# Performance work log

Hardware: AMD Instinct MI355X
Metric: run time of the kernel (lower is better)

Reference implementation:

```python
import jax, jax.numpy as jnp
import numpy as np

D = 12      # depth
C = 768     # embed_dim
NH = 12     # num_heads
P = 16      # patch_size
IMG = 224
G = IMG // P          # 14 patch grid
N = G * G + 1         # 197 tokens (CLS + patches)
WIN = 7               # window_size
NC = 1000             # num_classes
HID = 3072            # mlp hidden


def _local_mask():
    m = np.zeros((N, N), dtype=bool)
    m[0, :] = True
    m[:, 0] = True
    idx = np.arange(N - 1)
    r = idx // G
    c = idx % G
    half = WIN // 2
    m[1:, 1:] = (np.abs(r[:, None] - r[None, :]) <= half) & (np.abs(c[:, None] - c[None, :]) <= half)
    return jnp.asarray(m)

MASK = _local_mask()


def _ln(x, w, b, eps=1e-5):
    mu = x.mean(-1, keepdims=True)
    var = ((x - mu) ** 2).mean(-1, keepdims=True)
    return (x - mu) / jnp.sqrt(var + eps) * w + b


def setup_inputs() -> dict:
    key = jax.random.key(0)
    ks = jax.random.split(key, 16)
    s = jnp.float32(0.02)
    B = 32
    return {
        "x": jax.random.normal(ks[0], (B, 3, IMG, IMG), jnp.float32),
        "patch_w": jax.random.normal(ks[1], (C, 3, P, P), jnp.float32) * s,
        "patch_b": jnp.zeros((C,), jnp.float32),
        "cls_token": jax.random.normal(ks[2], (1, 1, C), jnp.float32) * s,
        "pos_embed": jax.random.normal(ks[3], (1, N, C), jnp.float32) * s,
        "ln1_w": jnp.ones((D, C), jnp.float32),
        "ln1_b": jnp.zeros((D, C), jnp.float32),
        "qkv_w": jax.random.normal(ks[4], (D, C, 3 * C), jnp.float32) * s,
        "proj_w": jax.random.normal(ks[5], (D, C, C), jnp.float32) * s,
        "proj_b": jnp.zeros((D, C), jnp.float32),
        "ln2_w": jnp.ones((D, C), jnp.float32),
        "ln2_b": jnp.zeros((D, C), jnp.float32),
        "mlp_w1": jax.random.normal(ks[6], (D, C, HID), jnp.float32) * s,
        "mlp_b1": jnp.zeros((D, HID), jnp.float32),
        "mlp_w2": jax.random.normal(ks[7], (D, HID, C), jnp.float32) * s,
        "mlp_b2": jnp.zeros((D, C), jnp.float32),
        "norm_w": jnp.ones((C,), jnp.float32),
        "norm_b": jnp.zeros((C,), jnp.float32),
        "head_w": jax.random.normal(ks[8], (C, NC), jnp.float32) * s,
        "head_b": jnp.zeros((NC,), jnp.float32),
    }


def reference(x, patch_w, patch_b, cls_token, pos_embed, ln1_w, ln1_b, qkv_w,
              proj_w, proj_b, ln2_w, ln2_b, mlp_w1, mlp_b1, mlp_w2, mlp_b2,
              norm_w, norm_b, head_w, head_b):
    B = x.shape[0]
    hd = C // NH
    scale = hd ** -0.5
    # Patch embed (Conv2d stride=kernel == non-overlapping patch matmul)
    xp = x.reshape(B, 3, G, P, G, P).transpose(0, 2, 4, 1, 3, 5).reshape(B, G * G, 3 * P * P)
    t = xp @ patch_w.reshape(C, 3 * P * P).T + patch_b
    t = jnp.concatenate([jnp.broadcast_to(cls_token, (B, 1, C)), t], axis=1) + pos_embed
    for i in range(D):
        h = _ln(t, ln1_w[i], ln1_b[i])
        qkv = (h @ qkv_w[i]).reshape(B, N, 3, NH, hd)
        q, k, v = qkv[:, :, 0], qkv[:, :, 1], qkv[:, :, 2]  # (B,N,NH,hd)
        attn = jnp.einsum('bqhd,bkhd->bhqk', q, k) * scale
        attn = jnp.where(MASK, attn, -jnp.inf)
        attn = jax.nn.softmax(attn, axis=-1)
        o = jnp.einsum('bhqk,bkhd->bqhd', attn, v).reshape(B, N, C)
        t = t + o @ proj_w[i] + proj_b[i]
        h = _ln(t, ln2_w[i], ln2_b[i])
        h = jax.nn.gelu(h @ mlp_w1[i] + mlp_b1[i], approximate=False)
        t = t + h @ mlp_w2[i] + mlp_b2[i]
    t = _ln(t, norm_w, norm_b)
    return t[:, 0] @ head_w + head_b
```

## Files before the change

### kernel.cpp

```cpp
#include <hip/hip_runtime.h>
#include <hip/hip_bf16.h>
#include <math.h>

#define Dn 12
#define Cc 768
#define NHh 12
#define HD 64
#define Gg 14
#define Nn_TOK 197
#define HID 3072
#define NC 1000
#define Bb 32

typedef __attribute__((ext_vector_type(8))) short short8;
typedef __attribute__((ext_vector_type(4))) float f32x4;

__device__ __forceinline__ ushort f2b(float v) {
    union { float f; unsigned u; } x; x.f = v;
    unsigned r = x.u + 0x7fff + ((x.u >> 16) & 1);
    return (ushort)(r >> 16);
}
__device__ __forceinline__ float b2f(ushort v) {
    union { unsigned u; float f; } x; x.u = ((unsigned)v) << 16; return x.f;
}
__device__ __forceinline__ void gld16(const void* g, void* s) {
    __builtin_amdgcn_global_load_lds(
        (const __attribute__((address_space(1))) void*)g,
        (__attribute__((address_space(3))) void*)s, 16, 0, 0);
}

__global__ void im2col_kernel(const float* __restrict__ x, ushort* __restrict__ xp) {
    size_t idx = (size_t)blockIdx.x * 256 + threadIdx.x;
    const size_t total = (size_t)Bb * 196 * 768;
    if (idx >= total) return;
    int j = idx % 768;
    size_t t0 = idx / 768;
    int g = t0 % 196;
    int b = t0 / 196;
    int ch = j / 256, rem = j % 256, pr = rem / 16, pc = rem % 16;
    int gr = g / Gg, gc = g % Gg;
    int row = gr * 16 + pr, col = gc * 16 + pc;
    xp[idx] = f2b(x[(((size_t)b * 3 + ch) * 224 + row) * 224 + col]);
}

__global__ void assemble_kernel(const float* __restrict__ pe, const float* __restrict__ cls,
                                const float* __restrict__ pos, float* __restrict__ t) {
    size_t idx = (size_t)blockIdx.x * 256 + threadIdx.x;
    const size_t total = (size_t)Bb * Nn_TOK * 768;
    if (idx >= total) return;
    int c = idx % 768;
    size_t r = idx / 768;
    int n = r % Nn_TOK, b = r / Nn_TOK;
    float v;
    if (n == 0) v = cls[c];
    else       v = pe[((size_t)b * 196 + (n - 1)) * 768 + c];
    t[idx] = v + pos[(size_t)n * 768 + c];
}

__global__ void cvt_kernel(const float* __restrict__ src, ushort* __restrict__ dst, int n) {
    int idx = blockIdx.x * 256 + threadIdx.x;
    if (idx < n) dst[idx] = f2b(src[idx]);
}

__global__ __launch_bounds__(256) void transpose_one(const float* __restrict__ src,
                                                     ushort* __restrict__ dst, int K, int N) {
    int k0 = blockIdx.x * 32, n0 = blockIdx.y * 32;
    __shared__ float tile[32][33];
    int tx = threadIdx.x & 31, ty = threadIdx.x >> 5;
    #pragma unroll
    for (int r = ty; r < 32; r += 8)
        if (k0 + r < K && n0 + tx < N)
            tile[r][tx] = src[(size_t)(k0 + r) * N + n0 + tx];
    __syncthreads();
    #pragma unroll
    for (int r = ty; r < 32; r += 8)
        if (n0 + r < N && k0 + tx < K)
            dst[(size_t)(n0 + r) * K + k0 + tx] = f2b(tile[tx][r]);
}

__global__ __launch_bounds__(256) void transpose4_kernel(
    const float* __restrict__ qkvw, const float* __restrict__ projw,
    const float* __restrict__ w1, const float* __restrict__ w2,
    ushort* __restrict__ dq, ushort* __restrict__ dp,
    ushort* __restrict__ d1, ushort* __restrict__ d2)
{
    int tile = blockIdx.x;
    const float* src; ushort* dst; int N, kt, nt;
    if (tile < 1728)      { src = qkvw; dst = dq; N = 2304; kt = tile / 72; nt = tile % 72; }
    else if (tile < 2304) { tile -= 1728; src = projw; dst = dp; N = 768; kt = tile / 24; nt = tile % 24; }
    else if (tile < 4608) { tile -= 2304; src = w1; dst = d1; N = 3072; kt = tile / 96; nt = tile % 96; }
    else                  { tile -= 4608; src = w2; dst = d2; N = 768; kt = tile / 24; nt = tile % 24; }
    int K = (dst == d2) ? 3072 : 768;
    int k0 = kt * 32, n0 = nt * 32;
    __shared__ float tilebuf[32][33];
    int tx = threadIdx.x & 31, ty = threadIdx.x >> 5;
    #pragma unroll
    for (int r = ty; r < 32; r += 8)
        tilebuf[r][tx] = src[(size_t)(k0 + r) * N + n0 + tx];
    __syncthreads();
    #pragma unroll
    for (int r = ty; r < 32; r += 8)
        dst[(size_t)(n0 + r) * K + k0 + tx] = f2b(tilebuf[tx][r]);
}

#define TM 128
#define TN 128
__global__ __launch_bounds__(256) void gemm_bf16(
    const ushort* __restrict__ A, const ushort* __restrict__ B,
    void* __restrict__ outp, const float* __restrict__ bias,
    const float* __restrict__ residual, int M, int N, int K, int flags)
{
    __shared__ ushort As[2][4][128][8];
    __shared__ ushort Bs[2][4][128][8];
    const int tid = threadIdx.x;
    const int wave = tid >> 6, lane = tid & 63;

    const int nwg = gridDim.x * gridDim.y;
    const int orig = blockIdx.y * gridDim.x + blockIdx.x;
    const int xcd = orig & 7, loc = orig >> 3;
    const int q8 = nwg >> 3, r8 = nwg & 7;
    const int swz = (xcd < r8 ? xcd * (q8 + 1) : r8 * (q8 + 1) + (xcd - r8) * q8) + loc;
    const int bx = swz % gridDim.x, by = swz / gridDim.x;

    const int br = by * TM, bc = bx * TN;
    const int wm = (wave >> 1) * 64, wn = (wave & 1) * 64;

    const int hA0 = tid >> 7, rA0 = tid & 127;
    const int hA1 = (tid + 256) >> 7;
    const ushort* pA0 = A + (size_t)min(br + rA0, M - 1) * K + hA0 * 8;
    const ushort* pA1 = A + (size_t)min(br + rA0, M - 1) * K + hA1 * 8;
    const ushort* pB0 = B + (size_t)min(bc + rA0, N - 1) * K + hA0 * 8;
    const ushort* pB1 = B + (size_t)min(bc + rA0, N - 1) * K + hA1 * 8;
    ushort* sA0 = &As[0][0][0][0] + (size_t)(wave * 64) * 8;
    ushort* sA1 = &As[0][0][0][0] + (size_t)(256 + wave * 64) * 8;
    ushort* sB0 = &Bs[0][0][0][0] + (size_t)(wave * 64) * 8;
    ushort* sB1 = &Bs[0][0][0][0] + (size_t)(256 + wave * 64) * 8;
    const size_t BUFO = 4096;

    f32x4 acc[4][4];
    #pragma unroll
    for (int i = 0; i < 4; ++i)
        #pragma unroll
        for (int j = 0; j < 4; ++j) acc[i][j] = (f32x4){0.f, 0.f, 0.f, 0.f};

    const int h = lane >> 4, m16 = lane & 15;
    const int nk = K >> 5;

    gld16(pA0, sA0); gld16(pA1, sA1);
    gld16(pB0, sB0); gld16(pB1, sB1);

    for (int kt = 0; kt < nk; ++kt) {
        const int cur = kt & 1;
        if (kt + 1 < nk) {
            const size_t ko = (size_t)(kt + 1) * 32;
            const size_t bo = (size_t)((kt + 1) & 1) * BUFO;
            gld16(pA0 + ko, sA0 + bo); gld16(pA1 + ko, sA1 + bo);
            gld16(pB0 + ko, sB0 + bo); gld16(pB1 + ko, sB1 + bo);
            asm volatile("s_waitcnt vmcnt(4)" ::: "memory");
        } else {
            asm volatile("s_waitcnt vmcnt(0)" ::: "memory");
        }
        __builtin_amdgcn_s_barrier();

        short8 af[4], bfr[4];
        #pragma unroll
        for (int i = 0; i < 4; ++i) af[i]  = *(const short8*)&As[cur][h][wm + i * 16 + m16][0];
        #pragma unroll
        for (int j = 0; j < 4; ++j) bfr[j] = *(const short8*)&Bs[cur][h][wn + j * 16 + m16][0];
        #pragma unroll
        for (int i = 0; i < 4; ++i)
            #pragma unroll
            for (int j = 0; j < 4; ++j)
                acc[i][j] = __builtin_amdgcn_mfma_f32_16x16x32_bf16(af[i], bfr[j], acc[i][j], 0, 0, 0);

        asm volatile("s_waitcnt lgkmcnt(0)" ::: "memory");
        __builtin_amdgcn_sched_barrier(0);
        __builtin_amdgcn_s_barrier();
    }

    const bool obf = (flags & 2) != 0, gelu = (flags & 1) != 0;
    const int q = lane >> 4, cx = lane & 15;
    #pragma unroll
    for (int j = 0; j < 4; ++j) {
        int gc = bc + wn + j * 16 + cx;
        if (gc >= N) continue;
        float bv = bias ? bias[gc] : 0.f;
        #pragma unroll
        for (int i = 0; i < 4; ++i) {
            #pragma unroll
            for (int r = 0; r < 4; ++r) {
                int gr = br + wm + i * 16 + q * 4 + r;
                if (gr >= M) continue;
                float v = acc[i][j][r] + bv;
                if (gelu) v = 0.5f * v * (1.f + erff(v * 0.70710678118654752f));
                size_t off = (size_t)gr * N + gc;
                if (residual) v += residual[off];
                if (obf) ((ushort*)outp)[off] = f2b(v);
                else     ((float*)outp)[off] = v;
            }
        }
    }
}

__global__ __launch_bounds__(256) void ln_kernel(
    const float* __restrict__ in, ushort* __restrict__ out,
    const float* __restrict__ w, const float* __restrict__ b, long in_stride)
{
    int row = blockIdx.x;
    const float* xr = in + (size_t)row * in_stride;
    ushort* orow = out + (size_t)row * 768;
    int tid = threadIdx.x;
    float vals[3];
    float s = 0.f, s2 = 0.f;
    #pragma unroll
    for (int l = 0; l < 3; ++l) {
        float v = xr[tid + l * 256];
        vals[l] = v; s += v; s2 += v * v;
    }
    __shared__ float sh[256];
    __shared__ float stats[2];
    sh[tid] = s; __syncthreads();
    for (int o = 128; o > 0; o >>= 1) { if (tid < o) sh[tid] += sh[tid + o]; __syncthreads(); }
    if (tid == 0) stats[0] = sh[0];
    __syncthreads();
    sh[tid] = s2; __syncthreads();
    for (int o = 128; o > 0; o >>= 1) { if (tid < o) sh[tid] += sh[tid + o]; __syncthreads(); }
    if (tid == 0) stats[1] = sh[0];
    __syncthreads();
    float mean = stats[0] * (1.f / 768.f);
    float var = stats[1] * (1.f / 768.f) - mean * mean;
    float rstd = rsqrtf(var + 1e-5f);
    #pragma unroll
    for (int l = 0; l < 3; ++l) {
        int c = tid + l * 256;
        orow[c] = f2b((vals[l] - mean) * rstd * w[c] + b[c]);
    }
}

#define VST 232
__global__ __launch_bounds__(256) void attn_kernel(
    const ushort* __restrict__ qkv, ushort* __restrict__ out)
{
    const int h = blockIdx.x, b = blockIdx.y, zs = blockIdx.z;
    __shared__ ushort Vsh[64][VST];
    __shared__ ushort Psh[4][16][VST];
    const int tid = threadIdx.x, wave = tid >> 6, lane = tid & 63;
    const size_t base = (size_t)b * Nn_TOK * 2304 + (size_t)h * 64;

    {
        short8* vf = (short8*)&Vsh[0][0];
        for (int i = tid; i < 64 * VST / 8; i += 256)
            vf[i] = (short8){0, 0, 0, 0, 0, 0, 0, 0};
    }
    __syncthreads();
    for (int idx = tid; idx < Nn_TOK * 32; idx += 256) {
        int n = idx >> 5, d2 = (idx & 31) * 2;
        unsigned u = *(const unsigned*)(qkv + base + 1536 + (size_t)n * 2304 + d2);
        Vsh[d2][n]     = (ushort)(u & 0xffffu);
        Vsh[d2 + 1][n] = (ushort)(u >> 16);
    }
    *(unsigned long long*)&Psh[wave][lane >> 2][208 + (lane & 3) * 4] = 0ull;
    __syncthreads();

    const int kcol = lane & 15, lhi = lane >> 4;
    int rk[14], ck[14]; bool kin[14], kwin[14];
    #pragma unroll
    for (int kt = 0; kt < 14; ++kt) {
        int k = kt * 16 + kcol;
        kin[kt]  = (k < Nn_TOK);
        kwin[kt] = (k >= 1) && (k < Nn_TOK);
        int km1 = k - 1;
        rk[kt] = km1 / 14;
        ck[kt] = km1 - rk[kt] * 14;
    }
    const bool kcls = (kcol == 0);

    const int tlo = zs ? 7 : 0, thi = zs ? 13 : 7;
    for (int qt = tlo + wave; qt < thi; qt += 4) {
        const int qbase = qt * 16;
        const int qrow = qbase + kcol;
        const ushort* qp = qkv + base + (size_t)min(qrow, Nn_TOK - 1) * 2304 + lhi * 8;
        const short8 qf0 = *(const short8*)qp;
        const short8 qf1 = *(const short8*)(qp + 32);

        f32x4 S[14];
        #pragma unroll
        for (int kt = 0; kt < 14; ++kt) {
            int krow = min(kt * 16 + kcol, Nn_TOK - 1);
            const ushort* kp = qkv + base + 768 + (size_t)krow * 2304 + lhi * 8;
            short8 kf0 = *(const short8*)kp;
            short8 kf1 = *(const short8*)(kp + 32);
            f32x4 s = (f32x4){0.f, 0.f, 0.f, 0.f};
            s = __builtin_amdgcn_mfma_f32_16x16x32_bf16(qf0, kf0, s, 0, 0, 0);
            s = __builtin_amdgcn_mfma_f32_16x16x32_bf16(qf1, kf1, s, 0, 0, 0);
            S[kt] = s;
        }

        int rq_[4], cq_[4]; bool qc_[4];
        #pragma unroll
        for (int r = 0; r < 4; ++r) {
            int q = qbase + lhi * 4 + r;
            qc_[r] = (q == 0);
            int qm1 = q - 1;
            rq_[r] = qm1 / 14;
            cq_[r] = qm1 - rq_[r] * 14;
        }
        #pragma unroll
        for (int kt = 0; kt < 14; ++kt)
            #pragma unroll
            for (int r = 0; r < 4; ++r) {
                unsigned dr = (unsigned)(rq_[r] - rk[kt] + 3);
                unsigned dc = (unsigned)(cq_[r] - ck[kt] + 3);
                bool ok = (kwin[kt] && dr <= 6u && dc <= 6u)
                          || (qc_[r] && kin[kt]) || (kt == 0 && kcls);
                S[kt][r] = ok ? S[kt][r] : -1e30f;
            }

        float mx[4] = {-1e30f, -1e30f, -1e30f, -1e30f};
        #pragma unroll
        for (int kt = 0; kt < 14; ++kt)
            #pragma unroll
            for (int r = 0; r < 4; ++r) mx[r] = fmaxf(mx[r], S[kt][r]);
        #pragma unroll
        for (int r = 0; r < 4; ++r) {
            #pragma unroll
            for (int o = 8; o > 0; o >>= 1) mx[r] = fmaxf(mx[r], __shfl_xor(mx[r], o));
        }
        float ls[4] = {0.f, 0.f, 0.f, 0.f};
        #pragma unroll
        for (int kt = 0; kt < 14; ++kt)
            #pragma unroll
            for (int r = 0; r < 4; ++r) {
                float p = __expf((S[kt][r] - mx[r]) * 0.125f);
                S[kt][r] = p; ls[r] += p;
            }
        #pragma unroll
        for (int r = 0; r < 4; ++r) {
            #pragma unroll
            for (int o = 8; o > 0; o >>= 1) ls[r] += __shfl_xor(ls[r], o);
            ls[r] = 1.f / ls[r];
        }

        #pragma unroll
        for (int kt = 0; kt < 13; ++kt)
            #pragma unroll
            for (int r = 0; r < 4; ++r)
                Psh[wave][lhi * 4 + r][kt * 16 + kcol] = f2b(S[kt][r] * ls[r]);

        f32x4 O[4];
        #pragma unroll
        for (int j = 0; j < 4; ++j) O[j] = (f32x4){0.f, 0.f, 0.f, 0.f};
        #pragma unroll
        for (int ks = 0; ks < 7; ++ks) {
            short8 pf = *(const short8*)&Psh[wave][kcol][ks * 32 + lhi * 8];
            #pragma unroll
            for (int j = 0; j < 4; ++j) {
                short8 vfr = *(const short8*)&Vsh[j * 16 + kcol][ks * 32 + lhi * 8];
                O[j] = __builtin_amdgcn_mfma_f32_16x16x32_bf16(pf, vfr, O[j], 0, 0, 0);
            }
        }

        #pragma unroll
        for (int r = 0; r < 4; ++r) {
            int q = qbase + lhi * 4 + r;
            if (q < Nn_TOK) {
                size_t orow = ((size_t)b * Nn_TOK + q) * 768 + (size_t)h * 64;
                #pragma unroll
                for (int j = 0; j < 4; ++j)
                    out[orow + j * 16 + kcol] = f2b(O[j][r]);
            }
        }
    }
}

extern "C" void kernel_launch(void* const* d_in, const int* in_sizes, int n_in,
                              void* d_out, int out_size, void* d_ws, size_t ws_size,
                              hipStream_t stream) {
    const float* x        = (const float*)d_in[0];
    const float* patch_w  = (const float*)d_in[1];
    const float* patch_b  = (const float*)d_in[2];
    const float* cls_tok  = (const float*)d_in[3];
    const float* pos_emb  = (const float*)d_in[4];
    const float* ln1_w    = (const float*)d_in[5];
    const float* ln1_b    = (const float*)d_in[6];
    const float* qkv_w    = (const float*)d_in[7];
    const float* proj_w   = (const float*)d_in[8];
    const float* proj_b   = (const float*)d_in[9];
    const float* ln2_w    = (const float*)d_in[10];
    const float* ln2_b    = (const float*)d_in[11];
    const float* mlp_w1   = (const float*)d_in[12];
    const float* mlp_b1   = (const float*)d_in[13];
    const float* mlp_w2   = (const float*)d_in[14];
    const float* mlp_b2   = (const float*)d_in[15];
    const float* norm_w   = (const float*)d_in[16];
    const float* norm_b   = (const float*)d_in[17];
    const float* head_w   = (const float*)d_in[18];
    const float* head_b   = (const float*)d_in[19];
    float* out = (float*)d_out;

    char* ws = (char*)d_ws;
    float*  t     = (float*)ws;
    float*  pbuf  = (float*)(ws + 19365888);
    ushort* abuf  = (ushort*)(ws + 38633472);
    ushort* qbuf  = (ushort*)(ws + 48316416);
    ushort* hbuf  = (ushort*)(ws + 77365248);
    ushort* wq    = (ushort*)(ws + 116097024);
    ushort* wp    = wq + 1769472;
    ushort* w1t   = wp + 589824;
    ushort* w2t   = w1t + 2359296;
    ushort* pwbuf = (ushort*)(ws + 130252800);
    ushort* hwbuf = (ushort*)(ws + 131432448);

    const int M_tok = Bb * Nn_TOK;

    {
        size_t total = (size_t)Bb * 196 * 768;
        im2col_kernel<<<dim3((total + 255) / 256), 256, 0, stream>>>(x, abuf);
    }
    cvt_kernel<<<dim3((589824 + 255) / 256), 256, 0, stream>>>(patch_w, pwbuf, 589824);
    transpose_one<<<dim3(24, 32), 256, 0, stream>>>(head_w, hwbuf, 768, NC);
    gemm_bf16<<<dim3(6, 49), 256, 0, stream>>>(abuf, pwbuf, pbuf, patch_b, nullptr, Bb * 196, Cc, Cc, 0);
    {
        size_t total = (size_t)M_tok * 768;
        assemble_kernel<<<dim3((total + 255) / 256), 256, 0, stream>>>(pbuf, cls_tok, pos_emb, t);
    }

    for (int i = 0; i < Dn; ++i) {
        transpose4_kernel<<<dim3(6912), 256, 0, stream>>>(
            qkv_w + (size_t)i * Cc * 3 * Cc, proj_w + (size_t)i * Cc * Cc,
            mlp_w1 + (size_t)i * Cc * HID, mlp_w2 + (size_t)i * HID * Cc,
            wq, wp, w1t, w2t);
        ln_kernel<<<dim3(M_tok), 256, 0, stream>>>(t, abuf, ln1_w + i * Cc, ln1_b + i * Cc, Cc);
        gemm_bf16<<<dim3(18, 50), 256, 0, stream>>>(abuf, wq, qbuf, nullptr, nullptr, M_tok, 3 * Cc, Cc, 2);
        attn_kernel<<<dim3(NHh, Bb, 2), 256, 0, stream>>>(qbuf, abuf);
        gemm_bf16<<<dim3(6, 50), 256, 0, stream>>>(abuf, wp, t, proj_b + i * Cc, t, M_tok, Cc, Cc, 0);
        ln_kernel<<<dim3(M_tok), 256, 0, stream>>>(t, abuf, ln2_w + i * Cc, ln2_b + i * Cc, Cc);
        gemm_bf16<<<dim3(24, 50), 256, 0, stream>>>(abuf, w1t, hbuf, mlp_b1 + i * HID, nullptr, M_tok, HID, Cc, 3);
        gemm_bf16<<<dim3(6, 50), 256, 0, stream>>>(hbuf, w2t, t, mlp_b2 + i * Cc, t, M_tok, Cc, HID, 0);
    }

    ln_kernel<<<dim3(Bb), 256, 0, stream>>>(t, abuf, norm_w, norm_b, (long)Nn_TOK * Cc);
    gemm_bf16<<<dim3(8, 1), 256, 0, stream>>>(abuf, hwbuf, out, head_b, nullptr, Bb, NC, Cc, 0);
}
```

Baseline: 5.474 ms.

## Replace 128x128 GEMM with templated 256xBN tile, K=64 steps, swizzled LDS

Replaces the 256-thread 128x128 bf16 MFMA GEMM with a templated 512-thread kernel. It uses 256-row tiles, 128- or 256-column tiles and a K step of 64, with an XOR-swizzled shared-memory layout and s_setprio around the MFMA bursts. The goals are more reuse per loaded tile, fewer barriers per K, and fewer LDS bank conflicts. In exchange it uses more registers and LDS, and some GEMMs launch fewer workgroups, for example 150 blocks for the N=768 GEMMs, which may underfill the GPU.

After: 4.817 ms. -12.0%, faster.

```diff
diff --git a/kernel.cpp b/kernel.cpp
--- a/kernel.cpp
+++ b/kernel.cpp
@@ -103,17 +103,22 @@
         dst[(size_t)(n0 + r) * K + k0 + tx] = f2b(tilebuf[tx][r]);
 }
 
-#define TM 128
-#define TN 128
-__global__ __launch_bounds__(256) void gemm_bf16(
+template<int BN>
+__global__ __launch_bounds__(512, 2) void gemm_t(
     const ushort* __restrict__ A, const ushort* __restrict__ B,
     void* __restrict__ outp, const float* __restrict__ bias,
     const float* __restrict__ residual, int M, int N, int K, int flags)
 {
-    __shared__ ushort As[2][4][128][8];
-    __shared__ ushort Bs[2][4][128][8];
+    constexpr int JF = BN / 64;
+    constexpr int BI = BN / 64;
+    constexpr int ATILE = 256 * 64;
+    constexpr int BTILE = BN * 64;
+    __shared__ ushort As[2 * ATILE];
+    __shared__ ushort Bs[2 * BTILE];
+
     const int tid = threadIdx.x;
     const int wave = tid >> 6, lane = tid & 63;
+    const int wr = wave >> 2, wc = wave & 3;
 
     const int nwg = gridDim.x * gridDim.y;
     const int orig = blockIdx.y * gridDim.x + blockIdx.x;
@@ -121,78 +126,98 @@
     const int q8 = nwg >> 3, r8 = nwg & 7;
     const int swz = (xcd < r8 ? xcd * (q8 + 1) : r8 * (q8 + 1) + (xcd - r8) * q8) + loc;
     const int bx = swz % gridDim.x, by = swz / gridDim.x;
-
-    const int br = by * TM, bc = bx * TN;
-    const int wm = (wave >> 1) * 64, wn = (wave & 1) * 64;
-
-    const int hA0 = tid >> 7, rA0 = tid & 127;
-    const int hA1 = (tid + 256) >> 7;
-    const ushort* pA0 = A + (size_t)min(br + rA0, M - 1) * K + hA0 * 8;
-    const ushort* pA1 = A + (size_t)min(br + rA0, M - 1) * K + hA1 * 8;
-    const ushort* pB0 = B + (size_t)min(bc + rA0, N - 1) * K + hA0 * 8;
-    const ushort* pB1 = B + (size_t)min(bc + rA0, N - 1) * K + hA1 * 8;
-    ushort* sA0 = &As[0][0][0][0] + (size_t)(wave * 64) * 8;
-    ushort* sA1 = &As[0][0][0][0] + (size_t)(256 + wave * 64) * 8;
-    ushort* sB0 = &Bs[0][0][0][0] + (size_t)(wave * 64) * 8;
-    ushort* sB1 = &Bs[0][0][0][0] + (size_t)(256 + wave * 64) * 8;
-    const size_t BUFO = 4096;
-
-    f32x4 acc[4][4];
-    #pragma unroll
-    for (int i = 0; i < 4; ++i)
-        #pragma unroll
-        for (int j = 0; j < 4; ++j) acc[i][j] = (f32x4){0.f, 0.f, 0.f, 0.f};
-
-    const int h = lane >> 4, m16 = lane & 15;
-    const int nk = K >> 5;
-
-    gld16(pA0, sA0); gld16(pA1, sA1);
-    gld16(pB0, sB0); gld16(pB1, sB1);
-
-    for (int kt = 0; kt < nk; ++kt) {
-        const int cur = kt & 1;
-        if (kt + 1 < nk) {
-            const size_t ko = (size_t)(kt + 1) * 32;
-            const size_t bo = (size_t)((kt + 1) & 1) * BUFO;
-            gld16(pA0 + ko, sA0 + bo); gld16(pA1 + ko, sA1 + bo);
-            gld16(pB0 + ko, sB0 + bo); gld16(pB1 + ko, sB1 + bo);
-            asm volatile("s_waitcnt vmcnt(4)" ::: "memory");
+    const int br = by * 256, bc = bx * BN;
+
+    const int srow = lane >> 3;
+    const int sswz = (lane & 7) ^ srow;
+    const ushort* pA[4]; const ushort* pB[4];
+    ushort* sA[4]; ushort* sB[4];
+    #pragma unroll
+    for (int i = 0; i < 4; ++i) {
+        int row = i * 64 + wave * 8 + srow;
+        pA[i] = A + (size_t)min(br + row, M - 1) * K + sswz * 8;
+        sA[i] = As + (i * 64 + wave * 8) * 64;
+    }
+    #pragma unroll
+    for (int i = 0; i < BI; ++i) {
+        int row = i * 64 + wave * 8 + srow;
+        pB[i] = B + (size_t)min(bc + row, N - 1) * K + sswz * 8;
+        sB[i] = Bs + (i * 64 + wave * 8) * 64;
+    }
+
+    f32x4 acc[8][JF];
+    #pragma unroll
+    for (int i = 0; i < 8; ++i)
+        #pragma unroll
+        for (int j = 0; j < JF; ++j) acc[i][j] = (f32x4){0.f, 0.f, 0.f, 0.f};
+
+    const int m16 = lane & 15, h = lane >> 4;
+    const int arow = (wr * 128 + m16) * 64;
+    const int brow = (wc * (BN / 4) + m16) * 64;
+    const int sx = m16 & 7;
+
+    const int nt = K >> 6;
+    #pragma unroll
+    for (int i = 0; i < 4; ++i) gld16(pA[i], sA[i]);
+    #pragma unroll
+    for (int i = 0; i < BI; ++i) gld16(pB[i], sB[i]);
+
+    for (int t = 0; t < nt; ++t) {
+        const int cur = t & 1;
+        if (t + 1 < nt) {
+            const size_t ko = (size_t)(t + 1) << 6;
+            const int nxt = cur ^ 1;
+            #pragma unroll
+            for (int i = 0; i < 4; ++i) gld16(pA[i] + ko, sA[i] + nxt * ATILE);
+            #pragma unroll
+            for (int i = 0; i < BI; ++i) gld16(pB[i] + ko, sB[i] + nxt * BTILE);
+            if constexpr (BN == 256) asm volatile("s_waitcnt vmcnt(8)" ::: "memory");
+            else                     asm volatile("s_waitcnt vmcnt(6)" ::: "memory");
         } else {
             asm volatile("s_waitcnt vmcnt(0)" ::: "memory");
         }
         __builtin_amdgcn_s_barrier();
-
-        short8 af[4], bfr[4];
-        #pragma unroll
-        for (int i = 0; i < 4; ++i) af[i]  = *(const short8*)&As[cur][h][wm + i * 16 + m16][0];
-        #pragma unroll
-        for (int j = 0; j < 4; ++j) bfr[j] = *(const short8*)&Bs[cur][h][wn + j * 16 + m16][0];
-        #pragma unroll
-        for (int i = 0; i < 4; ++i)
-            #pragma unroll
-            for (int j = 0; j < 4; ++j)
-                acc[i][j] = __builtin_amdgcn_mfma_f32_16x16x32_bf16(af[i], bfr[j], acc[i][j], 0, 0, 0);
-
+        __builtin_amdgcn_sched_barrier(0);
+
+        const ushort* Abase = As + cur * ATILE;
+        const ushort* Bbase = Bs + cur * BTILE;
+        #pragma unroll
+        for (int ks = 0; ks < 2; ++ks) {
+            const int slot = (((ks << 2) | h) ^ sx) << 3;
+            short8 af[8], bf[JF];
+            #pragma unroll
+            for (int i = 0; i < 8; ++i)
+                af[i] = *(const short8*)(Abase + arow + i * 1024 + slot);
+            #pragma unroll
+            for (int j = 0; j < JF; ++j)
+                bf[j] = *(const short8*)(Bbase + brow + j * 1024 + slot);
+            __builtin_amdgcn_s_setprio(1);
+            #pragma unroll
+            for (int i = 0; i < 8; ++i)
+                #pragma unroll
+                for (int j = 0; j < JF; ++j)
+                    acc[i][j] = __builtin_amdgcn_mfma_f32_16x16x32_bf16(af[i], bf[j], acc[i][j], 0, 0, 0);
+            __builtin_amdgcn_s_setprio(0);
+        }
         asm volatile("s_waitcnt lgkmcnt(0)" ::: "memory");
         __builtin_amdgcn_sched_barrier(0);
         __builtin_amdgcn_s_barrier();
     }
 
-    const bool obf = (flags & 2) != 0, gelu = (flags & 1) != 0;
-    const int q = lane >> 4, cx = lane & 15;
-    #pragma unroll
-    for (int j = 0; j < 4; ++j) {
-        int gc = bc + wn + j * 16 + cx;
+    const bool obf = (flags & 2) != 0, geluf = (flags & 1) != 0;
+    #pragma unroll
+    for (int j = 0; j < JF; ++j) {
+        int gc = bc + wc * (BN / 4) + j * 16 + m16;
         if (gc >= N) continue;
         float bv = bias ? bias[gc] : 0.f;
         #pragma unroll
-        for (int i = 0; i < 4; ++i) {
+        for (int i = 0; i < 8; ++i) {
             #pragma unroll
             for (int r = 0; r < 4; ++r) {
-                int gr = br + wm + i * 16 + q * 4 + r;
+                int gr = br + wr * 128 + i * 16 + h * 4 + r;
                 if (gr >= M) continue;
                 float v = acc[i][j][r] + bv;
-                if (gelu) v = 0.5f * v * (1.f + erff(v * 0.70710678118654752f));
+                if (geluf) v = 0.5f * v * (1.f + erff(v * 0.70710678118654752f));
                 size_t off = (size_t)gr * N + gc;
                 if (residual) v += residual[off];
                 if (obf) ((ushort*)outp)[off] = f2b(v);
@@ -419,7 +444,7 @@
     }
     cvt_kernel<<<dim3((589824 + 255) / 256), 256, 0, stream>>>(patch_w, pwbuf, 589824);
     transpose_one<<<dim3(24, 32), 256, 0, stream>>>(head_w, hwbuf, 768, NC);
-    gemm_bf16<<<dim3(6, 49), 256, 0, stream>>>(abuf, pwbuf, pbuf, patch_b, nullptr, Bb * 196, Cc, Cc, 0);
+    gemm_t<128><<<dim3(6, 25), 512, 0, stream>>>(abuf, pwbuf, pbuf, patch_b, nullptr, Bb * 196, Cc, Cc, 0);
     {
         size_t total = (size_t)M_tok * 768;
         assemble_kernel<<<dim3((total + 255) / 256), 256, 0, stream>>>(pbuf, cls_tok, pos_emb, t);
@@ -431,14 +456,14 @@
             mlp_w1 + (size_t)i * Cc * HID, mlp_w2 + (size_t)i * HID * Cc,
             wq, wp, w1t, w2t);
         ln_kernel<<<dim3(M_tok), 256, 0, stream>>>(t, abuf, ln1_w + i * Cc, ln1_b + i * Cc, Cc);
-        gemm_bf16<<<dim3(18, 50), 256, 0, stream>>>(abuf, wq, qbuf, nullptr, nullptr, M_tok, 3 * Cc, Cc, 2);
+        gemm_t<256><<<dim3(9, 25), 512, 0, stream>>>(abuf, wq, qbuf, nullptr, nullptr, M_tok, 3 * Cc, Cc, 2);
         attn_kernel<<<dim3(NHh, Bb, 2), 256, 0, stream>>>(qbuf, abuf);
-        gemm_bf16<<<dim3(6, 50), 256, 0, stream>>>(abuf, wp, t, proj_b + i * Cc, t, M_tok, Cc, Cc, 0);
+        gemm_t<128><<<dim3(6, 25), 512, 0, stream>>>(abuf, wp, t, proj_b + i * Cc, t, M_tok, Cc, Cc, 0);
         ln_kernel<<<dim3(M_tok), 256, 0, stream>>>(t, abuf, ln2_w + i * Cc, ln2_b + i * Cc, Cc);
-        gemm_bf16<<<dim3(24, 50), 256, 0, stream>>>(abuf, w1t, hbuf, mlp_b1 + i * HID, nullptr, M_tok, HID, Cc, 3);
-        gemm_bf16<<<dim3(6, 50), 256, 0, stream>>>(hbuf, w2t, t, mlp_b2 + i * Cc, t, M_tok, Cc, HID, 0);
+        gemm_t<256><<<dim3(12, 25), 512, 0, stream>>>(abuf, w1t, hbuf, mlp_b1 + i * HID, nullptr, M_tok, HID, Cc, 3);
+        gemm_t<128><<<dim3(6, 25), 512, 0, stream>>>(hbuf, w2t, t, mlp_b2 + i * Cc, t, M_tok, Cc, HID, 0);
     }
 
     ln_kernel<<<dim3(Bb), 256, 0, stream>>>(t, abuf, norm_w, norm_b, (long)Nn_TOK * Cc);
-    gemm_bf16<<<dim3(8, 1), 256, 0, stream>>>(abuf, hwbuf, out, head_b, nullptr, Bb, NC, Cc, 0);
-}
+    gemm_t<128><<<dim3(8, 1), 512, 0, stream>>>(abuf, hwbuf, out, head_b, nullptr, Bb, NC, Cc, 0);
+}
```
